# Optimization experiments

Measured on AMD Instinct MI355X. Metric: run time of the kernel, lower is better.

The kernel has to match this reference:

```python
import jax, jax.numpy as jnp
import numpy as np

B, N, H, NH = 4, 2048, 1024, 16
HD = H // NH  # head_dim = 64


def setup_inputs() -> dict:
    key = jax.random.key(0)
    k1, k2, k3 = jax.random.split(key, 3)
    s = 1.0 / np.sqrt(H)
    return {
        "x": jax.random.normal(k1, (B, N, H), dtype=jnp.float32),
        "w_qkv": jax.random.normal(k2, (3 * H, H), dtype=jnp.float32) * s,
        "b_qkv": jnp.zeros((3 * H,), dtype=jnp.float32),
        "w_out": jax.random.normal(k3, (H, H), dtype=jnp.float32) * s,
        "b_out": jnp.zeros((H,), dtype=jnp.float32),
    }


def reference(x, w_qkv, b_qkv, w_out, b_out):
    b, n, h = x.shape
    qkv = x @ w_qkv.T + b_qkv  # [b, n, 3h]
    q, k, v = jnp.split(qkv, 3, axis=-1)
    # [b, n, h] -> [b, nh, n, hd]
    def heads(t):
        return t.reshape(b, n, NH, HD).transpose(0, 2, 1, 3)
    q, k, v = heads(q), heads(k), heads(v)
    scale = HD ** -0.5
    dots = jnp.einsum('bhqd,bhkd->bhqk', q, k) * scale
    attn = jax.nn.softmax(dots, axis=-1)
    out = jnp.einsum('bhqk,bhkd->bhqd', attn, v)
    out = out.transpose(0, 2, 1, 3).reshape(b, n, h)
    return out @ w_out.T + b_out
```

## Files before the change

### kernel.cpp

```cpp
#include <hip/hip_runtime.h>

typedef __bf16 bf16x8 __attribute__((ext_vector_type(8)));
typedef float f32x4 __attribute__((ext_vector_type(4)));
typedef float f32x16 __attribute__((ext_vector_type(16)));
typedef unsigned int uint2v __attribute__((ext_vector_type(2)));

#define LOG2E 1.44269504088896340736f

#if __has_builtin(__builtin_amdgcn_exp2f)
#define EXP2(x) __builtin_amdgcn_exp2f(x)
#else
#define EXP2(x) exp2f(x)
#endif

static __device__ __forceinline__ unsigned short f2bf(float f) {
    unsigned int u = __builtin_bit_cast(unsigned int, f);
    u += 0x7fffu + ((u >> 16) & 1u);
    return (unsigned short)(u >> 16);
}

static __device__ __forceinline__ void plswap(unsigned int& a, unsigned int& b) {
#if __has_builtin(__builtin_amdgcn_permlane32_swap)
    uint2v r = __builtin_amdgcn_permlane32_swap(a, b, false, false);
    a = r.x; b = r.y;
#else
    asm("v_permlane32_swap_b32 %0, %1" : "+v"(a), "+v"(b));
#endif
}

static __device__ __forceinline__ float xhalf_add(float x) {
    unsigned int a = __builtin_bit_cast(unsigned int, x), b = a;
    plswap(a, b);
    return __builtin_bit_cast(float, a) + __builtin_bit_cast(float, b);
}

__global__ void cvt_kernel(const float* __restrict__ in, unsigned short* __restrict__ out, int n4) {
    int i = blockIdx.x * blockDim.x + threadIdx.x;
    int stride = gridDim.x * blockDim.x;
    for (; i < n4; i += stride) {
        float4 v = reinterpret_cast<const float4*>(in)[i];
        ushort4 o;
        o.x = f2bf(v.x); o.y = f2bf(v.y); o.z = f2bf(v.z); o.w = f2bf(v.w);
        reinterpret_cast<ushort4*>(out)[i] = o;
    }
}

template <int MODE>
__global__ __launch_bounds__(256, 2) void gemm_bt(const unsigned short* __restrict__ A,
                                                  const unsigned short* __restrict__ B,
                                                  const float* __restrict__ bias,
                                                  void* __restrict__ Cout,
                                                  int M, int N, int K) {
    __shared__ unsigned short SH[2][2][128 * 64];
    const int tid = threadIdx.x;
    const int w = tid >> 6, lane = tid & 63;
    const int wr = w >> 1, wc = w & 1;
    const int bm0 = blockIdx.y << 7, bn0 = blockIdx.x << 7;
    const int l15 = lane & 15, l4 = lane >> 4;

    const int srow = w * 8 + (lane >> 3);
    const int gch = (lane & 7) ^ (lane >> 3);

    f32x4 acc[4][4] = {};

    auto stage = [&](int buf, int kt) {
        const int k0 = kt << 6;
        #pragma unroll
        for (int i = 0; i < 4; ++i) {
            int row = i * 32 + srow;
            const unsigned short* ga = A + (size_t)(bm0 + row) * K + k0 + gch * 8;
            __builtin_amdgcn_global_load_lds(
                (const __attribute__((address_space(1))) void*)ga,
                (__attribute__((address_space(3))) void*)&SH[buf][0][i * 2048 + w * 512],
                16, 0, 0);
            const unsigned short* gb = B + (size_t)(bn0 + row) * K + k0 + gch * 8;
            __builtin_amdgcn_global_load_lds(
                (const __attribute__((address_space(1))) void*)gb,
                (__attribute__((address_space(3))) void*)&SH[buf][1][i * 2048 + w * 512],
                16, 0, 0);
        }
    };

    const int nk = K >> 6;
    stage(0, 0);
    __syncthreads();
    int buf = 0;
    for (int kt = 0; kt < nk; ++kt) {
        if (kt + 1 < nk) stage(buf ^ 1, kt + 1);
        const unsigned short* as = &SH[buf][0][0];
        const unsigned short* bs = &SH[buf][1][0];
        #pragma unroll
        for (int s = 0; s < 2; ++s) {
            bf16x8 af[4], bfr[4];
            #pragma unroll
            for (int t = 0; t < 4; ++t) {
                int rowa = wr * 64 + t * 16 + l15;
                int cha = (s * 4 + l4) ^ (rowa & 7);
                af[t] = *(const bf16x8*)&as[rowa * 64 + cha * 8];
                int rowb = wc * 64 + t * 16 + l15;
                int chb = (s * 4 + l4) ^ (rowb & 7);
                bfr[t] = *(const bf16x8*)&bs[rowb * 64 + chb * 8];
            }
            #pragma unroll
            for (int i = 0; i < 4; ++i)
                #pragma unroll
                for (int j = 0; j < 4; ++j)
                    acc[i][j] = __builtin_amdgcn_mfma_f32_16x16x32_bf16(af[i], bfr[j], acc[i][j], 0, 0, 0);
        }
        __syncthreads();
        buf ^= 1;
    }

    if (MODE == 0) {
        unsigned short* O = (unsigned short*)Cout;
        if (bn0 >= 2048) {
            unsigned short* T = &SH[0][0][0];
            __syncthreads();
            #pragma unroll
            for (int j = 0; j < 4; ++j) {
                int cl = wc * 64 + j * 16 + l15;
                float bv = bias[bn0 + cl];
                #pragma unroll
                for (int i = 0; i < 4; ++i) {
                    int nl = wr * 64 + i * 16 + l4 * 4;
                    ushort4 pk;
                    pk.x = f2bf(acc[i][j][0] + bv);
                    pk.y = f2bf(acc[i][j][1] + bv);
                    pk.z = f2bf(acc[i][j][2] + bv);
                    pk.w = f2bf(acc[i][j][3] + bv);
                    *(ushort4*)&T[cl * 136 + nl] = pk;
                }
            }
            __syncthreads();
            const int b = bm0 >> 11, n0 = bm0 & 2047;
            const int h0 = (bn0 >> 6) & 15;
            #pragma unroll
            for (int it = 0; it < 8; ++it) {
                int dl = it * 16 + (tid >> 4);
                int ch = tid & 15;
                uint4 val = *(const uint4*)&T[dl * 136 + ch * 8];
                size_t idx = (size_t)16777216 +
                             ((size_t)((b * 16 + (h0 + (dl >> 6))) * 64 + (dl & 63))) * 2048 +
                             n0 + ch * 8;
                *(uint4*)&O[idx] = val;
            }
        } else {
            #pragma unroll
            for (int j = 0; j < 4; ++j) {
                int col = bn0 + wc * 64 + j * 16 + l15;
                float bv = bias[col];
                int which = col >> 10;
                int h = (col >> 6) & 15;
                int d = col & 63;
                #pragma unroll
                for (int i = 0; i < 4; ++i) {
                    #pragma unroll
                    for (int r = 0; r < 4; ++r) {
                        int row = bm0 + wr * 64 + i * 16 + l4 * 4 + r;
                        int b = row >> 11, n = row & 2047;
                        float v = acc[i][j][r] + bv;
                        size_t idx;
                        if (which == 0) { v *= 0.125f * LOG2E; idx = ((size_t)((b * 16 + h) * 2048 + n)) * 64 + d; }
                        else { idx = (size_t)8388608 + ((size_t)((b * 16 + h) * 2048 + n)) * 64 + d; }
                        O[idx] = f2bf(v);
                    }
                }
            }
        }
    } else {
        float* C = (float*)Cout;
        #pragma unroll
        for (int j = 0; j < 4; ++j) {
            int col = bn0 + wc * 64 + j * 16 + l15;
            float bv = bias[col];
            #pragma unroll
            for (int i = 0; i < 4; ++i) {
                #pragma unroll
                for (int r = 0; r < 4; ++r) {
                    int row = bm0 + wr * 64 + i * 16 + l4 * 4 + r;
                    C[(size_t)row * N + col] = acc[i][j][r] + bv;
                }
            }
        }
    }
}

__global__ __launch_bounds__(256, 2) void attn_kernel(const unsigned short* __restrict__ qkv,
                                                      unsigned short* __restrict__ out) {
    __shared__ unsigned short Klds[2][4096];
    __shared__ unsigned short Vlds[2][4096];

    const int tid = threadIdx.x;
    const int w = tid >> 6, lane = tid & 63;
    const int ql = lane & 31;
    const int hi = lane >> 5;
    const int id = blockIdx.x;
    const int bh = id & 63;
    const int qt = id >> 6;
    const size_t SEC = 8388608;

    const unsigned short* Q  = qkv + (size_t)bh * (2048 * 64);
    const unsigned short* Kp = qkv + SEC + (size_t)bh * (2048 * 64);
    const unsigned short* Vt = qkv + 2 * SEC + (size_t)bh * (64 * 2048);

    const int q0 = qt * 256 + w * 64;

    bf16x8 qbA[4], qbB[4];
    #pragma unroll
    for (int c = 0; c < 4; ++c) {
        qbA[c] = *(const bf16x8*)&Q[(size_t)(q0 + ql) * 64 + c * 16 + hi * 8];
        qbB[c] = *(const bf16x8*)&Q[(size_t)(q0 + 32 + ql) * 64 + c * 16 + hi * 8];
    }

    f32x16 oA0 = {}, oA1 = {}, oB0 = {}, oB1 = {};
    float lsA = 0.f, lsB = 0.f;

    const int sri = lane >> 3;
    const int sch = lane & 7;

    auto stage = [&](int buf, int tile) {
        const int kb = tile * 64;
        #pragma unroll
        for (int i = 0; i < 2; ++i) {
            const int r = w * 16 + i * 8 + sri;
            const int c = sch ^ (r & 7);
            const unsigned short* gk = Kp + (size_t)(kb + r) * 64 + c * 8;
            __builtin_amdgcn_global_load_lds(
                (const __attribute__((address_space(1))) void*)gk,
                (__attribute__((address_space(3))) void*)&Klds[buf][w * 1024 + i * 512],
                16, 0, 0);
            const unsigned short* gv = Vt + (size_t)r * 2048 + kb + c * 8;
            __builtin_amdgcn_global_load_lds(
                (const __attribute__((address_space(1))) void*)gv,
                (__attribute__((address_space(3))) void*)&Vlds[buf][w * 1024 + i * 512],
                16, 0, 0);
        }
    };

    auto softmax_block = [&](f32x16& s0, f32x16& s1, float& lsum,
                             bf16x8 (&p0)[2], bf16x8 (&p1)[2]) {
        #pragma unroll
        for (int r = 0; r < 16; ++r) s0[r] = EXP2(s0[r]);
        #pragma unroll
        for (int r = 0; r < 16; ++r) s1[r] = EXP2(s1[r]);
        float u0 = ((s0[0] + s0[1]) + (s0[2] + s0[3])) + ((s0[4] + s0[5]) + (s0[6] + s0[7]));
        float u1 = ((s0[8] + s0[9]) + (s0[10] + s0[11])) + ((s0[12] + s0[13]) + (s0[14] + s0[15]));
        float u2 = ((s1[0] + s1[1]) + (s1[2] + s1[3])) + ((s1[4] + s1[5]) + (s1[6] + s1[7]));
        float u3 = ((s1[8] + s1[9]) + (s1[10] + s1[11])) + ((s1[12] + s1[13]) + (s1[14] + s1[15]));
        float rs = (u0 + u1) + (u2 + u3);
        lsum += xhalf_add(rs);
        #pragma unroll
        for (int g = 0; g < 2; ++g) {
            unsigned int x0, x1, x2, x3;
            asm("v_cvt_pk_bf16_f32 %0, %1, %2" : "=v"(x0) : "v"(s0[8*g + 0]), "v"(s0[8*g + 1]));
            asm("v_cvt_pk_bf16_f32 %0, %1, %2" : "=v"(x1) : "v"(s0[8*g + 2]), "v"(s0[8*g + 3]));
            asm("v_cvt_pk_bf16_f32 %0, %1, %2" : "=v"(x2) : "v"(s0[8*g + 4]), "v"(s0[8*g + 5]));
            asm("v_cvt_pk_bf16_f32 %0, %1, %2" : "=v"(x3) : "v"(s0[8*g + 6]), "v"(s0[8*g + 7]));
            plswap(x0, x2);
            plswap(x1, x3);
            uint4 wds; wds.x = x0; wds.y = x1; wds.z = x2; wds.w = x3;
            p0[g] = __builtin_bit_cast(bf16x8, wds);
        }
        #pragma unroll
        for (int g = 0; g < 2; ++g) {
            unsigned int x0, x1, x2, x3;
            asm("v_cvt_pk_bf16_f32 %0, %1, %2" : "=v"(x0) : "v"(s1[8*g + 0]), "v"(s1[8*g + 1]));
            asm("v_cvt_pk_bf16_f32 %0, %1, %2" : "=v"(x1) : "v"(s1[8*g + 2]), "v"(s1[8*g + 3]));
            asm("v_cvt_pk_bf16_f32 %0, %1, %2" : "=v"(x2) : "v"(s1[8*g + 4]), "v"(s1[8*g + 5]));
            asm("v_cvt_pk_bf16_f32 %0, %1, %2" : "=v"(x3) : "v"(s1[8*g + 6]), "v"(s1[8*g + 7]));
            plswap(x0, x2);
            plswap(x1, x3);
            uint4 wds; wds.x = x0; wds.y = x1; wds.z = x2; wds.w = x3;
            p1[g] = __builtin_bit_cast(bf16x8, wds);
        }
    };

    stage(0, 0);
    __syncthreads();

    for (int t = 0; t < 32; ++t) {
        const int cur = t & 1;
        if (t + 1 < 32) stage(cur ^ 1, t + 1);

        bf16x8 k0[4], k1[4];
        #pragma unroll
        for (int mf = 0; mf < 4; ++mf) {
            int c0 = ((mf * 2 + hi) ^ (ql & 7));
            k0[mf] = *(const bf16x8*)&Klds[cur][ql * 64 + c0 * 8];
            k1[mf] = *(const bf16x8*)&Klds[cur][(32 + ql) * 64 + c0 * 8];
        }

        f32x16 sA0 = {}, sA1 = {};
        #pragma unroll
        for (int mf = 0; mf < 4; ++mf)
            sA0 = __builtin_amdgcn_mfma_f32_32x32x16_bf16(k0[mf], qbA[mf], sA0, 0, 0, 0);
        #pragma unroll
        for (int mf = 0; mf < 4; ++mf)
            sA1 = __builtin_amdgcn_mfma_f32_32x32x16_bf16(k1[mf], qbA[mf], sA1, 0, 0, 0);
        f32x16 sB0 = {}, sB1 = {};
        #pragma unroll
        for (int mf = 0; mf < 4; ++mf)
            sB0 = __builtin_amdgcn_mfma_f32_32x32x16_bf16(k0[mf], qbB[mf], sB0, 0, 0, 0);
        #pragma unroll
        for (int mf = 0; mf < 4; ++mf)
            sB1 = __builtin_amdgcn_mfma_f32_32x32x16_bf16(k1[mf], qbB[mf], sB1, 0, 0, 0);

        bf16x8 v0[4], v1[4];
        #pragma unroll
        for (int ks = 0; ks < 4; ++ks) {
            int c0 = ((ks * 2 + hi) ^ (ql & 7));
            v0[ks] = *(const bf16x8*)&Vlds[cur][ql * 64 + c0 * 8];
            v1[ks] = *(const bf16x8*)&Vlds[cur][(32 + ql) * 64 + c0 * 8];
        }

        bf16x8 pA0[2], pA1[2], pB0[2], pB1[2];
        softmax_block(sA0, sA1, lsA, pA0, pA1);
        softmax_block(sB0, sB1, lsB, pB0, pB1);

        oA0 = __builtin_amdgcn_mfma_f32_32x32x16_bf16(v0[0], pA0[0], oA0, 0, 0, 0);
        oA0 = __builtin_amdgcn_mfma_f32_32x32x16_bf16(v0[1], pA0[1], oA0, 0, 0, 0);
        oA0 = __builtin_amdgcn_mfma_f32_32x32x16_bf16(v0[2], pA1[0], oA0, 0, 0, 0);
        oA0 = __builtin_amdgcn_mfma_f32_32x32x16_bf16(v0[3], pA1[1], oA0, 0, 0, 0);
        oA1 = __builtin_amdgcn_mfma_f32_32x32x16_bf16(v1[0], pA0[0], oA1, 0, 0, 0);
        oA1 = __builtin_amdgcn_mfma_f32_32x32x16_bf16(v1[1], pA0[1], oA1, 0, 0, 0);
        oA1 = __builtin_amdgcn_mfma_f32_32x32x16_bf16(v1[2], pA1[0], oA1, 0, 0, 0);
        oA1 = __builtin_amdgcn_mfma_f32_32x32x16_bf16(v1[3], pA1[1], oA1, 0, 0, 0);
        oB0 = __builtin_amdgcn_mfma_f32_32x32x16_bf16(v0[0], pB0[0], oB0, 0, 0, 0);
        oB0 = __builtin_amdgcn_mfma_f32_32x32x16_bf16(v0[1], pB0[1], oB0, 0, 0, 0);
        oB0 = __builtin_amdgcn_mfma_f32_32x32x16_bf16(v0[2], pB1[0], oB0, 0, 0, 0);
        oB0 = __builtin_amdgcn_mfma_f32_32x32x16_bf16(v0[3], pB1[1], oB0, 0, 0, 0);
        oB1 = __builtin_amdgcn_mfma_f32_32x32x16_bf16(v1[0], pB0[0], oB1, 0, 0, 0);
        oB1 = __builtin_amdgcn_mfma_f32_32x32x16_bf16(v1[1], pB0[1], oB1, 0, 0, 0);
        oB1 = __builtin_amdgcn_mfma_f32_32x32x16_bf16(v1[2], pB1[0], oB1, 0, 0, 0);
        oB1 = __builtin_amdgcn_mfma_f32_32x32x16_bf16(v1[3], pB1[1], oB1, 0, 0, 0);

        __syncthreads();
    }

    const int b = bh >> 4, h = bh & 15;
    {
        const float inv = 1.0f / lsA;
        const int n = q0 + ql;
        unsigned short* obase = out + ((size_t)(b * 2048 + n)) * 1024 + h * 64;
        #pragma unroll
        for (int g = 0; g < 4; ++g) {
            int d0 = 8 * g + 4 * hi;
            ushort4 w0, w1;
            w0.x = f2bf(oA0[4 * g + 0] * inv);
            w0.y = f2bf(oA0[4 * g + 1] * inv);
            w0.z = f2bf(oA0[4 * g + 2] * inv);
            w0.w = f2bf(oA0[4 * g + 3] * inv);
            *(ushort4*)(obase + d0) = w0;
            w1.x = f2bf(oA1[4 * g + 0] * inv);
            w1.y = f2bf(oA1[4 * g + 1] * inv);
            w1.z = f2bf(oA1[4 * g + 2] * inv);
            w1.w = f2bf(oA1[4 * g + 3] * inv);
            *(ushort4*)(obase + 32 + d0) = w1;
        }
    }
    {
        const float inv = 1.0f / lsB;
        const int n = q0 + 32 + ql;
        unsigned short* obase = out + ((size_t)(b * 2048 + n)) * 1024 + h * 64;
        #pragma unroll
        for (int g = 0; g < 4; ++g) {
            int d0 = 8 * g + 4 * hi;
            ushort4 w0, w1;
            w0.x = f2bf(oB0[4 * g + 0] * inv);
            w0.y = f2bf(oB0[4 * g + 1] * inv);
            w0.z = f2bf(oB0[4 * g + 2] * inv);
            w0.w = f2bf(oB0[4 * g + 3] * inv);
            *(ushort4*)(obase + d0) = w0;
            w1.x = f2bf(oB1[4 * g + 0] * inv);
            w1.y = f2bf(oB1[4 * g + 1] * inv);
            w1.z = f2bf(oB1[4 * g + 2] * inv);
            w1.w = f2bf(oB1[4 * g + 3] * inv);
            *(ushort4*)(obase + 32 + d0) = w1;
        }
    }
}

extern "C" void kernel_launch(void* const* d_in, const int* in_sizes, int n_in,
                              void* d_out, int out_size, void* d_ws, size_t ws_size,
                              hipStream_t stream) {
    (void)in_sizes; (void)n_in; (void)out_size; (void)ws_size;
    const float* x     = (const float*)d_in[0];
    const float* w_qkv = (const float*)d_in[1];
    const float* b_qkv = (const float*)d_in[2];
    const float* w_out = (const float*)d_in[3];
    const float* b_out = (const float*)d_in[4];

    unsigned short* ws = (unsigned short*)d_ws;
    unsigned short* xb    = ws;
    unsigned short* wqkvb = ws + 8388608;
    unsigned short* woutb = ws + 11534336;
    unsigned short* qkvb  = ws + 12582912;

    cvt_kernel<<<dim3(2048), dim3(256), 0, stream>>>(x, xb, 8388608 / 4);
    cvt_kernel<<<dim3(1024), dim3(256), 0, stream>>>(w_qkv, wqkvb, 3145728 / 4);
    cvt_kernel<<<dim3(512),  dim3(256), 0, stream>>>(w_out, woutb, 1048576 / 4);

    gemm_bt<0><<<dim3(24, 64), dim3(256), 0, stream>>>(xb, wqkvb, b_qkv, (void*)qkvb, 8192, 3072, 1024);

    attn_kernel<<<dim3(512), dim3(256), 0, stream>>>(qkvb, xb);

    gemm_bt<1><<<dim3(8, 64), dim3(256), 0, stream>>>(xb, woutb, b_out, d_out, 8192, 1024, 1024);
}
```

Baseline: 180.4 us.

## Widen GEMM tiles to 128x256 with 512 threads and split-K pipelined staging

```diff
diff --git a/kernel.cpp b/kernel.cpp
--- a/kernel.cpp
+++ b/kernel.cpp
@@ -46,123 +46,145 @@
 }
 
 template <int MODE>
-__global__ __launch_bounds__(256, 2) void gemm_bt(const unsigned short* __restrict__ A,
+__global__ __launch_bounds__(512, 2) void gemm256(const unsigned short* __restrict__ A,
                                                   const unsigned short* __restrict__ B,
                                                   const float* __restrict__ bias,
                                                   void* __restrict__ Cout,
-                                                  int M, int N, int K) {
-    __shared__ unsigned short SH[2][2][128 * 64];
+                                                  int M, int N, int K, int nbx) {
+    __shared__ unsigned short SMEM[49152];
+
     const int tid = threadIdx.x;
     const int w = tid >> 6, lane = tid & 63;
-    const int wr = w >> 1, wc = w & 1;
-    const int bm0 = blockIdx.y << 7, bn0 = blockIdx.x << 7;
+    const int wr = w >> 2, wc = w & 3;
     const int l15 = lane & 15, l4 = lane >> 4;
 
-    const int srow = w * 8 + (lane >> 3);
-    const int gch = (lane & 7) ^ (lane >> 3);
+    const int cpx = gridDim.x >> 3;
+    const int swzb = (blockIdx.x & 7) * cpx + (blockIdx.x >> 3);
+    const int bx = swzb % nbx, by = swzb / nbx;
+    const int bm0 = by << 7, bn0 = bx << 8;
+
+    const int strow = tid >> 2;
+    const int stc = tid & 3;
 
     f32x4 acc[4][4] = {};
 
-    auto stage = [&](int buf, int kt) {
-        const int k0 = kt << 6;
-        #pragma unroll
-        for (int i = 0; i < 4; ++i) {
-            int row = i * 32 + srow;
-            const unsigned short* ga = A + (size_t)(bm0 + row) * K + k0 + gch * 8;
+    auto stage_slice = [&](int buf, int kt, int s) {
+        const int k0 = (kt << 6) + s * 32;
+        {
+            int row = strow;
+            int c = stc ^ (row & 3) ^ ((row >> 2) & 3);
+            const unsigned short* g = A + (size_t)(bm0 + row) * K + k0 + c * 8;
             __builtin_amdgcn_global_load_lds(
-                (const __attribute__((address_space(1))) void*)ga,
-                (__attribute__((address_space(3))) void*)&SH[buf][0][i * 2048 + w * 512],
+                (const __attribute__((address_space(1))) void*)g,
+                (__attribute__((address_space(3))) void*)&SMEM[buf * 8192 + s * 4096 + tid * 8],
                 16, 0, 0);
-            const unsigned short* gb = B + (size_t)(bn0 + row) * K + k0 + gch * 8;
+        }
+        #pragma unroll
+        for (int i = 0; i < 2; ++i) {
+            int row = i * 128 + strow;
+            int c = stc ^ (row & 3) ^ ((row >> 2) & 3);
+            const unsigned short* g = B + (size_t)(bn0 + row) * K + k0 + c * 8;
             __builtin_amdgcn_global_load_lds(
-                (const __attribute__((address_space(1))) void*)gb,
-                (__attribute__((address_space(3))) void*)&SH[buf][1][i * 2048 + w * 512],
+                (const __attribute__((address_space(1))) void*)g,
+                (__attribute__((address_space(3))) void*)&SMEM[16384 + buf * 16384 + s * 8192 + i * 4096 + tid * 8],
                 16, 0, 0);
         }
     };
 
     const int nk = K >> 6;
-    stage(0, 0);
+    stage_slice(0, 0, 0);
+    stage_slice(0, 0, 1);
+
+    const int rA0 = wr * 64 + l15;
+    const int rB0 = wc * 64 + l15;
+
+    for (int kt = 0; kt < nk; ++kt) {
+        const int p = kt & 1;
+        #pragma unroll
+        for (int s = 0; s < 2; ++s) {
+            if (kt == nk - 1 && s == 1) {
+                asm volatile("s_waitcnt vmcnt(0)" ::: "memory");
+            } else {
+                asm volatile("s_waitcnt vmcnt(3)" ::: "memory");
+            }
+            __builtin_amdgcn_s_barrier();
+            __builtin_amdgcn_sched_barrier(0);
+            if (kt + 1 < nk) stage_slice(p ^ 1, kt + 1, s);
+
+            bf16x8 af[4], bfr[4];
+            #pragma unroll
+            for (int fr = 0; fr < 4; ++fr) {
+                int row = rA0 + fr * 16;
+                int c = l4 ^ (row & 3) ^ ((row >> 2) & 3);
+                af[fr] = *(const bf16x8*)&SMEM[p * 8192 + s * 4096 + row * 32 + c * 8];
+            }
+            #pragma unroll
+            for (int nj = 0; nj < 4; ++nj) {
+                int row = rB0 + nj * 16;
+                int c = l4 ^ (row & 3) ^ ((row >> 2) & 3);
+                bfr[nj] = *(const bf16x8*)&SMEM[16384 + p * 16384 + s * 8192 + row * 32 + c * 8];
+            }
+            __builtin_amdgcn_s_setprio(1);
+            #pragma unroll
+            for (int fr = 0; fr < 4; ++fr)
+                #pragma unroll
+                for (int nj = 0; nj < 4; ++nj)
+                    acc[fr][nj] = __builtin_amdgcn_mfma_f32_16x16x32_bf16(af[fr], bfr[nj], acc[fr][nj], 0, 0, 0);
+            __builtin_amdgcn_s_setprio(0);
+            __builtin_amdgcn_sched_barrier(0);
+        }
+    }
     __syncthreads();
-    int buf = 0;
-    for (int kt = 0; kt < nk; ++kt) {
-        if (kt + 1 < nk) stage(buf ^ 1, kt + 1);
-        const unsigned short* as = &SH[buf][0][0];
-        const unsigned short* bs = &SH[buf][1][0];
-        #pragma unroll
-        for (int s = 0; s < 2; ++s) {
-            bf16x8 af[4], bfr[4];
-            #pragma unroll
-            for (int t = 0; t < 4; ++t) {
-                int rowa = wr * 64 + t * 16 + l15;
-                int cha = (s * 4 + l4) ^ (rowa & 7);
-                af[t] = *(const bf16x8*)&as[rowa * 64 + cha * 8];
-                int rowb = wc * 64 + t * 16 + l15;
-                int chb = (s * 4 + l4) ^ (rowb & 7);
-                bfr[t] = *(const bf16x8*)&bs[rowb * 64 + chb * 8];
-            }
-            #pragma unroll
-            for (int i = 0; i < 4; ++i)
-                #pragma unroll
-                for (int j = 0; j < 4; ++j)
-                    acc[i][j] = __builtin_amdgcn_mfma_f32_16x16x32_bf16(af[i], bfr[j], acc[i][j], 0, 0, 0);
-        }
-        __syncthreads();
-        buf ^= 1;
-    }
 
     if (MODE == 0) {
         unsigned short* O = (unsigned short*)Cout;
         if (bn0 >= 2048) {
-            unsigned short* T = &SH[0][0][0];
-            __syncthreads();
-            #pragma unroll
-            for (int j = 0; j < 4; ++j) {
-                int cl = wc * 64 + j * 16 + l15;
+            unsigned short* T = &SMEM[0];
+            #pragma unroll
+            for (int nj = 0; nj < 4; ++nj) {
+                int cl = wc * 64 + nj * 16 + l15;
                 float bv = bias[bn0 + cl];
                 #pragma unroll
-                for (int i = 0; i < 4; ++i) {
-                    int nl = wr * 64 + i * 16 + l4 * 4;
+                for (int fr = 0; fr < 4; ++fr) {
+                    int nl = wr * 64 + fr * 16 + l4 * 4;
                     ushort4 pk;
-                    pk.x = f2bf(acc[i][j][0] + bv);
-                    pk.y = f2bf(acc[i][j][1] + bv);
-                    pk.z = f2bf(acc[i][j][2] + bv);
-                    pk.w = f2bf(acc[i][j][3] + bv);
+                    pk.x = f2bf(acc[fr][nj][0] + bv);
+                    pk.y = f2bf(acc[fr][nj][1] + bv);
+                    pk.z = f2bf(acc[fr][nj][2] + bv);
+                    pk.w = f2bf(acc[fr][nj][3] + bv);
                     *(ushort4*)&T[cl * 136 + nl] = pk;
                 }
             }
             __syncthreads();
             const int b = bm0 >> 11, n0 = bm0 & 2047;
-            const int h0 = (bn0 >> 6) & 15;
             #pragma unroll
             for (int it = 0; it < 8; ++it) {
-                int dl = it * 16 + (tid >> 4);
-                int ch = tid & 15;
-                uint4 val = *(const uint4*)&T[dl * 136 + ch * 8];
+                int flat = it * 512 + tid;
+                int cl = flat >> 4, ch = flat & 15;
+                uint4 val = *(const uint4*)&T[cl * 136 + ch * 8];
+                int col = bn0 + cl;
+                int h = (col >> 6) & 15, d = col & 63;
                 size_t idx = (size_t)16777216 +
-                             ((size_t)((b * 16 + (h0 + (dl >> 6))) * 64 + (dl & 63))) * 2048 +
-                             n0 + ch * 8;
+                             ((size_t)((b * 16 + h) * 64 + d)) * 2048 + n0 + ch * 8;
                 *(uint4*)&O[idx] = val;
             }
         } else {
             #pragma unroll
-            for (int j = 0; j < 4; ++j) {
-                int col = bn0 + wc * 64 + j * 16 + l15;
+            for (int nj = 0; nj < 4; ++nj) {
+                int col = bn0 + wc * 64 + nj * 16 + l15;
                 float bv = bias[col];
                 int which = col >> 10;
-                int h = (col >> 6) & 15;
-                int d = col & 63;
+                int h = (col >> 6) & 15, d = col & 63;
+                float scale = (which == 0) ? 0.125f * LOG2E : 1.0f;
+                size_t base = (which == 0) ? (size_t)0 : (size_t)8388608;
                 #pragma unroll
-                for (int i = 0; i < 4; ++i) {
+                for (int fr = 0; fr < 4; ++fr) {
                     #pragma unroll
                     for (int r = 0; r < 4; ++r) {
-                        int row = bm0 + wr * 64 + i * 16 + l4 * 4 + r;
+                        int row = bm0 + wr * 64 + fr * 16 + l4 * 4 + r;
                         int b = row >> 11, n = row & 2047;
-                        float v = acc[i][j][r] + bv;
-                        size_t idx;
-                        if (which == 0) { v *= 0.125f * LOG2E; idx = ((size_t)((b * 16 + h) * 2048 + n)) * 64 + d; }
-                        else { idx = (size_t)8388608 + ((size_t)((b * 16 + h) * 2048 + n)) * 64 + d; }
-                        O[idx] = f2bf(v);
+                        float v = (acc[fr][nj][r] + bv) * scale;
+                        O[base + ((size_t)((b * 16 + h) * 2048 + n)) * 64 + d] = f2bf(v);
                     }
                 }
             }
@@ -170,15 +192,15 @@
     } else {
         float* C = (float*)Cout;
         #pragma unroll
-        for (int j = 0; j < 4; ++j) {
-            int col = bn0 + wc * 64 + j * 16 + l15;
+        for (int nj = 0; nj < 4; ++nj) {
+            int col = bn0 + wc * 64 + nj * 16 + l15;
             float bv = bias[col];
             #pragma unroll
-            for (int i = 0; i < 4; ++i) {
+            for (int fr = 0; fr < 4; ++fr) {
                 #pragma unroll
                 for (int r = 0; r < 4; ++r) {
-                    int row = bm0 + wr * 64 + i * 16 + l4 * 4 + r;
-                    C[(size_t)row * N + col] = acc[i][j][r] + bv;
+                    int row = bm0 + wr * 64 + fr * 16 + l4 * 4 + r;
+                    C[(size_t)row * N + col] = acc[fr][nj][r] + bv;
                 }
             }
         }
@@ -400,9 +422,9 @@
     cvt_kernel<<<dim3(1024), dim3(256), 0, stream>>>(w_qkv, wqkvb, 3145728 / 4);
     cvt_kernel<<<dim3(512),  dim3(256), 0, stream>>>(w_out, woutb, 1048576 / 4);
 
-    gemm_bt<0><<<dim3(24, 64), dim3(256), 0, stream>>>(xb, wqkvb, b_qkv, (void*)qkvb, 8192, 3072, 1024);
+    gemm256<0><<<dim3(768), dim3(512), 0, stream>>>(xb, wqkvb, b_qkv, (void*)qkvb, 8192, 3072, 1024, 12);
 
     attn_kernel<<<dim3(512), dim3(256), 0, stream>>>(qkvb, xb);
 
-    gemm_bt<1><<<dim3(8, 64), dim3(256), 0, stream>>>(xb, woutb, b_out, d_out, 8192, 1024, 1024);
-}
+    gemm256<1><<<dim3(256), dim3(512), 0, stream>>>(xb, woutb, b_out, d_out, 8192, 1024, 1024, 4);
+}
```

Result: slower. 189.1 us (+4.8%).
